# Optimization experiments

Hardware: AMD Instinct MI355X
Metric: run time of the kernel (lower is better)

The kernel has to match this reference:

```python
import jax, jax.numpy as jnp
import numpy as np
import math

SF = 2      # sr_forward
SP = 2      # sr_prior
LAM = 0.05  # lam


def _cubic(x):
    ax = np.abs(x); ax2 = ax * ax; ax3 = ax2 * ax
    return (1.5 * ax3 - 2.5 * ax2 + 1.0) * (ax <= 1) + \
           (-0.5 * ax3 + 2.5 * ax2 - 4.0 * ax + 2.0) * ((ax > 1) & (ax <= 2))


def _weights_indices(in_len, out_len, scale, antialiasing):
    # matlab-style bicubic resample weights (KAIR imresize), computed statically in numpy
    kw = 4.0
    if scale < 1 and antialiasing:
        kw = kw / scale
    x = np.arange(1, out_len + 1, dtype=np.float64)
    u = x / scale + 0.5 * (1.0 - 1.0 / scale)
    left = np.floor(u - kw / 2)
    P = int(math.ceil(kw)) + 2
    ind = left[:, None] + np.arange(P, dtype=np.float64)[None, :]
    dist = u[:, None] - ind
    w = scale * _cubic(dist * scale) if (scale < 1 and antialiasing) else _cubic(dist)
    w = w / w.sum(axis=1, keepdims=True)
    nz = (w == 0).sum(axis=0)
    if nz[0] != 0:
        ind = ind[:, 1:1 + P - 2]; w = w[:, 1:1 + P - 2]
    if nz[-1] != 0:
        ind = ind[:, 0:P - 2]; w = w[:, 0:P - 2]
    sym_s = int(-ind.min() + 1)
    sym_e = int(ind.max() - in_len)
    ind0 = (ind + sym_s - 1).astype(np.int64)  # 0-based into symmetrically padded axis
    return w, ind0, sym_s, sym_e


def imresize(x, scale, antialiasing):
    # x: (C, H, W); faithful matlab bicubic with symmetric boundary padding
    C, H, W = x.shape
    oH, oW = int(math.ceil(H * scale)), int(math.ceil(W * scale))
    wH, iH, sHs, sHe = _weights_indices(H, oH, scale, antialiasing)
    wW, iW, sWs, sWe = _weights_indices(W, oW, scale, antialiasing)
    xp = jnp.pad(x, ((0, 0), (sHs, max(sHe, 0)), (0, 0)), mode='symmetric')
    y = jnp.einsum('chpw,hp->chw', xp[:, iH, :], jnp.asarray(wH, x.dtype))
    yp = jnp.pad(y, ((0, 0), (0, 0), (sWs, max(sWe, 0))), mode='symmetric')
    return jnp.einsum('chwp,wp->chw', yp[:, :, iW], jnp.asarray(wW, x.dtype))


def wrap_conv(x, k):
    # ndimage.convolve(x_HWC, k[...,None], mode='wrap') per channel; k odd-sized (K,K)
    kh, kw = k.shape
    ph, pw = kh // 2, kw // 2
    xp = jnp.pad(x, ((0, 0), (ph, kh - 1 - ph), (pw, kw - 1 - pw)), mode='wrap')
    kf = jnp.flip(k, (0, 1)).astype(x.dtype)[None, None]  # true convolution = corr with flipped kernel
    out = jax.lax.conv_general_dilated(xp[:, None], kf, (1, 1), 'VALID')
    return out[:, 0]


def shift_pixel(x, sf):
    # bilinear (scipy interp2d linear) shift by (sf-1)/2 toward upper-left, clipped at borders
    C, H, W = x.shape
    s = (sf - 1) * 0.5
    yv = np.clip(np.arange(H) + s, 0, H - 1)
    xv = np.clip(np.arange(W) + s, 0, W - 1)
    y0 = np.floor(yv).astype(np.int64); y1 = np.minimum(y0 + 1, H - 1)
    x0 = np.floor(xv).astype(np.int64); x1 = np.minimum(x0 + 1, W - 1)
    wy = jnp.asarray(yv - y0, x.dtype)[None, :, None]
    wx = jnp.asarray(xv - x0, x.dtype)[None, None, :]
    t = x[:, y0, :] * (1 - wy) + x[:, y1, :] * wy
    return t[:, :, x0] * (1 - wx) + t[:, :, x1] * wx


def setup_inputs() -> dict:
    key = jax.random.key(0)
    im = jax.random.normal(key, (1, 3, 2048, 2048), dtype=jnp.float32)
    # 25x25 Gaussian blur kernel (typical SISR forward kernel), normalized to sum 1
    g = np.arange(25) - 12.0
    g = np.exp(-(g ** 2) / (2 * 2.6 ** 2))
    k = np.outer(g, g); k = k / k.sum()
    kernel = jnp.asarray(k, jnp.float32)
    return {"im": im, "kernel": kernel}


def reference(im, kernel):
    x = im[0]                                        # (C, H, W); batch must be 1
    ax = wrap_conv(x, kernel)                        # A: wrap blur
    ax = imresize(ax, 1.0 / SF, False)               # A: downsample (no antialias)
    atax = imresize(ax, float(SF), False)            # A^T: upsample
    atax = wrap_conv(atax, jnp.flip(kernel, (0, 1))) # A^T: conv with flipped kernel
    atax = shift_pixel(atax, SF)                     # A^T: half-pixel alignment shift
    hx = imresize(x, 1.0 / SP, True)                 # H: antialiased downsample
    hthx = imresize(hx, float(SP), True)             # H^T: upsample
    return atax[None] + LAM * hthx[None]             # (1, C, H, W)
```

## Files before the change

kernel.cpp:

```cpp
#include <hip/hip_runtime.h>
#include <math.h>

namespace {

constexpr int W = 2048, H = 2048, NC = 3, HALF = 1024;
constexpr size_t HWSZ = (size_t)W * H;
constexpr size_t MQ = (size_t)HALF * HALF;
constexpr size_t M2 = 2 * MQ;
constexpr float LAM = 0.05f;

__device__ __forceinline__ int refl(int i, int n) {
    return i < 0 ? -1 - i : (i >= n ? 2 * n - 1 - i : i);
}

__global__ void prep(const float* __restrict__ k, float* __restrict__ cf) {
    if (threadIdx.x != 0) return;
    float g[25];
#pragma unroll
    for (int p = 0; p < 25; ++p) { g[p] = sqrtf(k[p * 25 + p]); cf[p] = g[p]; }
    float hw[26];
    hw[0] = 0.5f * g[0];
#pragma unroll
    for (int t = 1; t < 25; ++t) hw[t] = 0.5f * (g[t] + g[t - 1]);
    hw[25] = 0.5f * g[24];
#pragma unroll
    for (int t = 0; t < 26; ++t) cf[32 + t] = hw[t];
#pragma unroll
    for (int d = 0; d < 28; ++d) {
        float s = 0.f;
        if (d < 25) s = fmaf(-0.0625f, g[d], s);
        if (d >= 1 && d <= 25) s = fmaf(0.5625f, g[d - 1], s);
        if (d >= 2 && d <= 26) s = fmaf(0.5625f, g[d - 2], s);
        if (d >= 3) s = fmaf(-0.0625f, g[d - 3], s);
        cf[64 + d] = s;
    }
    const float WE4[4] = {-0.0234375f, 0.2265625f, 0.8671875f, -0.0703125f};
    float C0[17], C1[17];
#pragma unroll
    for (int m = 0; m < 17; ++m) { C0[m] = 0.f; C1[m] = 0.f; }
#pragma unroll
    for (int p = 0; p < 2; ++p) {
#pragma unroll
        for (int t = 0; t < 26; ++t) {
            int r = p - 12 + t;
            int fl = (r + 64) / 2 - 32;
            int e = (r + 64) & 1;
#pragma unroll
            for (int b = 0; b < 4; ++b) {
                int m = fl + e + b - 2 + 8;
                float wub = e ? WE4[3 - b] : WE4[b];
                float add = hw[t] * wub;
                if (p == 0) C0[m] += add;
                else C1[m] += add;
            }
        }
    }
#pragma unroll
    for (int m = 0; m < 17; ++m) { cf[96 + m] = C0[m]; cf[128 + m] = C1[m]; }
}

__global__ __launch_bounds__(256) void front(const float* __restrict__ x,
                                             float* __restrict__ d1,
                                             float* __restrict__ hx,
                                             const float* __restrict__ cf) {
    __shared__ float xs[90][97];
    __shared__ float th[90][33];
    int b = blockIdx.x;
    int tx = b & 31, ty = (b >> 5) & 31, c = b >> 10;
    int tid = threadIdx.x;
    const int r0 = 64 * ty - 13;
    const int c0 = 64 * tx - 16;
    const float* xb = x + (size_t)c * HWSZ;
    {
        int lane8 = tid & 7;
        int rsub = tid >> 3;
#pragma unroll
        for (int rp = 0; rp < 3; ++rp) {
            int r = rp * 32 + rsub;
            if (r < 90) {
                const float* xr = xb + (size_t)((r0 + r) & 2047) * W;
#pragma unroll
                for (int g4 = 0; g4 < 3; ++g4) {
                    int cc = g4 * 8 + lane8;
                    float4 v = *(const float4*)(xr + ((c0 + 4 * cc) & 2047));
                    xs[r][4 * cc + 0] = v.x; xs[r][4 * cc + 1] = v.y;
                    xs[r][4 * cc + 2] = v.z; xs[r][4 * cc + 3] = v.w;
                }
            }
        }
    }
    float g[25], cw[28];
#pragma unroll
    for (int p = 0; p < 25; ++p) g[p] = cf[p];
#pragma unroll
    for (int d = 0; d < 28; ++d) cw[d] = cf[64 + d];
    const bool BROW = (ty == 0 || ty == 31);
    const bool BCOL = (tx == 0 || tx == 31);
    __syncthreads();

    const float WA[8] = {-0.01171875f, -0.03515625f, 0.11328125f, 0.43359375f,
                         0.43359375f,  0.11328125f,  -0.03515625f, -0.01171875f};
    const int ob_r0 = 64 * ty - 3, ob_c0 = 64 * tx - 3;
    for (int idx = tid; idx < 560; idx += 256) {
        int rr = idx >> 3, q = idx & 7;
        int lr = BROW ? (refl(ob_r0 + rr, H) - r0) : (rr + 10);
        const float* xr = &xs[lr][0];
        float a0 = 0.f, a1 = 0.f, a2 = 0.f, a3 = 0.f;
        if (!BCOL) {
            const float* xp = xr + 13 + 8 * q;
#pragma unroll
            for (int u = 0; u < 14; ++u) {
                float v = xp[u];
                if (u < 8) a0 = fmaf(WA[u], v, a0);
                if (u >= 2 && u < 10) a1 = fmaf(WA[u - 2], v, a1);
                if (u >= 4 && u < 12) a2 = fmaf(WA[u - 4], v, a2);
                if (u >= 6) a3 = fmaf(WA[u - 6], v, a3);
            }
        } else {
#pragma unroll
            for (int u = 0; u < 14; ++u) {
                float v = xr[refl(ob_c0 + 8 * q + u, W) - c0];
                if (u < 8) a0 = fmaf(WA[u], v, a0);
                if (u >= 2 && u < 10) a1 = fmaf(WA[u - 2], v, a1);
                if (u >= 4 && u < 12) a2 = fmaf(WA[u - 4], v, a2);
                if (u >= 6) a3 = fmaf(WA[u - 6], v, a3);
            }
        }
        th[rr][4 * q + 0] = a0;
        th[rr][4 * q + 1] = a1;
        th[rr][4 * q + 2] = a2;
        th[rr][4 * q + 3] = a3;
    }
    __syncthreads();
    {
        int oc = tid & 31, og = tid >> 5;
        float a0 = 0.f, a1 = 0.f, a2 = 0.f, a3 = 0.f;
#pragma unroll
        for (int u = 0; u < 14; ++u) {
            float v = th[8 * og + u][oc];
            if (u < 8) a0 = fmaf(WA[u], v, a0);
            if (u >= 2 && u < 10) a1 = fmaf(WA[u - 2], v, a1);
            if (u >= 4 && u < 12) a2 = fmaf(WA[u - 4], v, a2);
            if (u >= 6) a3 = fmaf(WA[u - 6], v, a3);
        }
        float* hp = hx + (size_t)c * MQ + (size_t)(32 * ty + 4 * og) * HALF + 32 * tx + oc;
        hp[0] = a0; hp[HALF] = a1; hp[2 * HALF] = a2; hp[3 * HALF] = a3;
    }
    __syncthreads();

    for (int idx = tid; idx < 720; idx += 256) {
        int r = idx >> 3, q = idx & 7;
        const float* xp = &xs[r][8 * q + 3];
        float a0 = 0.f, a1 = 0.f, a2 = 0.f, a3 = 0.f;
#pragma unroll
        for (int u = 0; u < 34; ++u) {
            float v = xp[u];
            if (u < 28) a0 = fmaf(cw[u], v, a0);
            if (u >= 2 && u < 30) a1 = fmaf(cw[u - 2], v, a1);
            if (u >= 4 && u < 32) a2 = fmaf(cw[u - 4], v, a2);
            if (u >= 6) a3 = fmaf(cw[u - 6], v, a3);
        }
        th[r][4 * q + 0] = a0;
        th[r][4 * q + 1] = a1;
        th[r][4 * q + 2] = a2;
        th[r][4 * q + 3] = a3;
    }
    __syncthreads();
    if (tx == 0) {
        for (int r = tid; r < 90; r += 256) {
            float b0 = 0.f, b1 = 0.f, b2 = 0.f;
#pragma unroll
            for (int p = 0; p < 25; ++p) {
                b0 = fmaf(g[p], xs[r][p + 4], b0);
                b1 = fmaf(g[p], xs[r][p + 5], b1);
                b2 = fmaf(g[p], xs[r][p + 6], b2);
            }
            th[r][0] = 0.5f * b0 + 0.5625f * b1 - 0.0625f * b2;
        }
    }
    if (tx == 31) {
        for (int r = tid; r < 90; r += 256) {
            float b0 = 0.f, b1 = 0.f, b2 = 0.f;
#pragma unroll
            for (int p = 0; p < 25; ++p) {
                b0 = fmaf(g[p], xs[r][p + 65], b0);
                b1 = fmaf(g[p], xs[r][p + 66], b1);
                b2 = fmaf(g[p], xs[r][p + 67], b2);
            }
            th[r][31] = -0.0625f * b0 + 0.5625f * b1 + 0.5f * b2;
        }
    }
    __syncthreads();

    {
        int oc = tid & 31, og = tid >> 5;
        float a0 = 0.f, a1 = 0.f, a2 = 0.f, a3 = 0.f;
#pragma unroll
        for (int u = 0; u < 34; ++u) {
            float v = th[8 * og + u][oc];
            if (u < 28) a0 = fmaf(cw[u], v, a0);
            if (u >= 2 && u < 30) a1 = fmaf(cw[u - 2], v, a1);
            if (u >= 4 && u < 32) a2 = fmaf(cw[u - 4], v, a2);
            if (u >= 6) a3 = fmaf(cw[u - 6], v, a3);
        }
        float av[4] = {a0, a1, a2, a3};
        if (ty == 0 && og == 0) {
            float b0 = 0.f, b1 = 0.f, b2 = 0.f;
#pragma unroll
            for (int p = 0; p < 25; ++p) {
                b0 = fmaf(g[p], th[1 + p][oc], b0);
                b1 = fmaf(g[p], th[2 + p][oc], b1);
                b2 = fmaf(g[p], th[3 + p][oc], b2);
            }
            av[0] = 0.5f * b0 + 0.5625f * b1 - 0.0625f * b2;
        }
        if (ty == 31 && og == 7) {
            float b0 = 0.f, b1 = 0.f, b2 = 0.f;
#pragma unroll
            for (int p = 0; p < 25; ++p) {
                b0 = fmaf(g[p], th[62 + p][oc], b0);
                b1 = fmaf(g[p], th[63 + p][oc], b1);
                b2 = fmaf(g[p], th[64 + p][oc], b2);
            }
            av[3] = -0.0625f * b0 + 0.5625f * b1 + 0.5f * b2;
        }
        float* dp = d1 + (size_t)c * MQ + (size_t)(32 * ty + 4 * og) * HALF + 32 * tx + oc;
#pragma unroll
        for (int k = 0; k < 4; ++k) dp[(size_t)k * HALF] = av[k];
    }
}

__global__ __launch_bounds__(256) void aK(const float* __restrict__ d1,
                                          float* __restrict__ m1,
                                          const float* __restrict__ cf) {
    int b = blockIdx.x;
    int tid = threadIdx.x;
    if (b < 256 * NC) {
        int ib = b & 255, c = b >> 8;
        if (ib < 2 || ib > 253) return;
        float C0[17], C1[17];
#pragma unroll
        for (int m = 0; m < 17; ++m) { C0[m] = cf[96 + m]; C1[m] = cf[128 + m]; }
        int i0 = 8 * ib, q0 = 4 * ib;
        const float* dp = d1 + ((size_t)c * MQ + (size_t)(q0 - 8) * HALF + 4 * tid);
        float4 acc[8];
#pragma unroll
        for (int k = 0; k < 8; ++k) acc[k] = make_float4(0.f, 0.f, 0.f, 0.f);
#pragma unroll
        for (int d = 0; d < 20; ++d) {
            float4 v = *(const float4*)(dp + (size_t)d * HALF);
#pragma unroll
            for (int k = 0; k < 8; ++k) {
                int m = d - (k >> 1);
                if (m >= 0 && m < 17) {
                    float wgt = (k & 1) ? C1[m] : C0[m];
                    acc[k].x = fmaf(wgt, v.x, acc[k].x);
                    acc[k].y = fmaf(wgt, v.y, acc[k].y);
                    acc[k].z = fmaf(wgt, v.z, acc[k].z);
                    acc[k].w = fmaf(wgt, v.w, acc[k].w);
                }
            }
        }
        float* mp = m1 + (size_t)c * M2 + (size_t)i0 * HALF + 4 * tid;
#pragma unroll
        for (int k = 0; k < 8; ++k) *(float4*)(mp + (size_t)k * HALF) = acc[k];
    } else {
        int bid = b - 256 * NC;
        int ri = bid & 31, c = bid >> 5;
        int i = ri < 16 ? ri : 2016 + ri;
        float g[25], hw[26];
#pragma unroll
        for (int p = 0; p < 25; ++p) g[p] = cf[p];
#pragma unroll
        for (int t = 0; t < 26; ++t) hw[t] = cf[32 + t];
        const float WE4[4] = {-0.0234375f, 0.2265625f, 0.8671875f, -0.0703125f};
        bool cl = (i == 2047);
        const float* db = d1 + (size_t)c * MQ + 4 * tid;
        float4 a = make_float4(0.f, 0.f, 0.f, 0.f);
#pragma unroll
        for (int t = 0; t < 26; ++t) {
            float wgt = cl ? (t < 25 ? g[t] : 0.f) : hw[t];
            int ip = (i - 12 + t) & 2047;
            int e = ip & 1, qq = (ip >> 1) + e - 2;
            float4 uv = make_float4(0.f, 0.f, 0.f, 0.f);
#pragma unroll
            for (int bq = 0; bq < 4; ++bq) {
                float wu = e ? WE4[3 - bq] : WE4[bq];
                int rr = refl(qq + bq, HALF);
                float4 v = *(const float4*)(db + (size_t)rr * HALF);
                uv.x = fmaf(wu, v.x, uv.x);
                uv.y = fmaf(wu, v.y, uv.y);
                uv.z = fmaf(wu, v.z, uv.z);
                uv.w = fmaf(wu, v.w, uv.w);
            }
            a.x = fmaf(wgt, uv.x, a.x);
            a.y = fmaf(wgt, uv.y, a.y);
            a.z = fmaf(wgt, uv.z, a.z);
            a.w = fmaf(wgt, uv.w, a.w);
        }
        *(float4*)(m1 + (size_t)c * M2 + (size_t)i * HALF + 4 * tid) = a;
    }
}

__global__ __launch_bounds__(256) void bK(const float* __restrict__ m1,
                                          const float* __restrict__ hx,
                                          float* __restrict__ out,
                                          const float* __restrict__ cf) {
    __shared__ float mr[4][1040];
    __shared__ float hv[4][1040];
    int b = blockIdx.x;
    int tid = threadIdx.x;
    const float WE4[4] = {-0.0234375f, 0.2265625f, 0.8671875f, -0.0703125f};
    if (b < 512 * NC) {
        int rb = b & 511, c = b >> 9;
        float C0[17], C1[17];
#pragma unroll
        for (int m = 0; m < 17; ++m) { C0[m] = cf[96 + m]; C1[m] = cf[128 + m]; }
        int i0 = 4 * rb;
        const float* mb = m1 + (size_t)c * M2 + (size_t)i0 * HALF;
#pragma unroll
        for (int r = 0; r < 4; ++r) {
            float4 v = *(const float4*)(mb + (size_t)r * HALF + 4 * tid);
            *(float4*)&mr[r][8 + 4 * tid] = v;
        }
        const float* hb = hx + (size_t)c * MQ;
        int q2 = 2 * rb;
#pragma unroll
        for (int k = 0; k < 4; ++k) {
            float4 a = make_float4(0.f, 0.f, 0.f, 0.f);
#pragma unroll
            for (int aq = 0; aq < 4; ++aq) {
                float wu = (k & 1) ? WE4[3 - aq] : WE4[aq];
                int row = refl(q2 - 2 + (k >> 1) + (k & 1) + aq, HALF);
                float4 v = *(const float4*)(hb + (size_t)row * HALF + 4 * tid);
                a.x = fmaf(wu, v.x, a.x);
                a.y = fmaf(wu, v.y, a.y);
                a.z = fmaf(wu, v.z, a.z);
                a.w = fmaf(wu, v.w, a.w);
            }
            *(float4*)&hv[k][4 + 4 * tid] = a;
            if (tid == 0) { hv[k][3] = a.x; hv[k][2] = a.y; }
            if (tid == 255) { hv[k][4 + 1024] = a.w; hv[k][4 + 1025] = a.z; }
        }
        __syncthreads();
        bool dostore = (tid >= 2 && tid <= 253);
        float* ob = out + (size_t)c * HWSZ + (size_t)i0 * W + 8 * tid;
#pragma unroll
        for (int r = 0; r < 4; ++r) {
            float w[20];
#pragma unroll
            for (int q5 = 0; q5 < 5; ++q5)
                *(float4*)&w[4 * q5] = *(const float4*)&mr[r][4 * tid + 4 * q5];
            float wv[12];
#pragma unroll
            for (int q3 = 0; q3 < 3; ++q3)
                *(float4*)&wv[4 * q3] = *(const float4*)&hv[r][4 * tid + 4 * q3];
            float res[8];
#pragma unroll
            for (int s = 0; s < 8; ++s) {
                int h = s >> 1;
                float a = 0.f;
#pragma unroll
                for (int m = 0; m < 17; ++m)
                    a = fmaf((s & 1) ? C1[m] : C0[m], w[h + m], a);
                float uh = 0.f;
#pragma unroll
                for (int bq = 0; bq < 4; ++bq)
                    uh = fmaf((s & 1) ? WE4[3 - bq] : WE4[bq], wv[h + (s & 1) + 2 + bq], uh);
                res[s] = fmaf(LAM, uh, a);
            }
            if (dostore) {
                *(float4*)(ob + (size_t)r * W) = make_float4(res[0], res[1], res[2], res[3]);
                *(float4*)(ob + (size_t)r * W + 4) = make_float4(res[4], res[5], res[6], res[7]);
            }
        }
    } else {
        int bid = b - 512 * NC;
        int rg = bid & 255, c = bid >> 8;
        int i = 8 * rg + (tid >> 5);
        int cc = tid & 31;
        int j = cc < 16 ? cc : 2016 + cc;
        float g[25], hw[26];
#pragma unroll
        for (int p = 0; p < 25; ++p) g[p] = cf[p];
#pragma unroll
        for (int t = 0; t < 26; ++t) hw[t] = cf[32 + t];
        const float* mrow = m1 + (size_t)c * M2 + (size_t)i * HALF;
        bool cl = (j == 2047);
        float val = 0.f;
#pragma unroll
        for (int t = 0; t < 26; ++t) {
            float wgt = cl ? (t < 25 ? g[t] : 0.f) : hw[t];
            int jp = (j - 12 + t) & 2047;
            int e = jp & 1;
            int qq = (jp >> 1) + e - 2;
            float uh = 0.f;
#pragma unroll
            for (int bq = 0; bq < 4; ++bq)
                uh = fmaf(e ? WE4[3 - bq] : WE4[bq], mrow[refl(qq + bq, HALF)], uh);
            val = fmaf(wgt, uh, val);
        }
        const float* hb = hx + (size_t)c * MQ;
        int qi = (i >> 1) + (i & 1) - 2;
        int qj = (j >> 1) + (j & 1) - 2;
        float hval = 0.f;
#pragma unroll
        for (int aq = 0; aq < 4; ++aq) {
            const float* hr = hb + (size_t)refl(qi + aq, HALF) * HALF;
            float rowa = (i & 1) ? WE4[3 - aq] : WE4[aq];
            float s = 0.f;
#pragma unroll
            for (int bq = 0; bq < 4; ++bq)
                s = fmaf((j & 1) ? WE4[3 - bq] : WE4[bq], hr[refl(qj + bq, HALF)], s);
            hval = fmaf(rowa, s, hval);
        }
        out[(size_t)c * HWSZ + (size_t)i * W + j] = fmaf(LAM, hval, val);
    }
}

}

extern "C" void kernel_launch(void* const* d_in, const int* in_sizes, int n_in,
                              void* d_out, int out_size, void* d_ws, size_t ws_size,
                              hipStream_t stream) {
    (void)in_sizes; (void)n_in; (void)out_size; (void)ws_size;
    const float* x = (const float*)d_in[0];
    const float* k = (const float*)d_in[1];
    float* ws = (float*)d_ws;
    float* out = (float*)d_out;

    float* hxp = ws;
    float* d1 = hxp + 3 * MQ;
    float* m1 = d1 + 3 * MQ;
    float* cf = m1 + 3 * M2;

    hipLaunchKernelGGL(prep, dim3(1), dim3(32), 0, stream, k, cf);
    hipLaunchKernelGGL(front, dim3(32 * 32 * NC), dim3(256), 0, stream, x, d1, hxp, cf);
    hipLaunchKernelGGL(aK, dim3(256 * NC + 32 * NC), dim3(256), 0, stream, d1, m1, cf);
    hipLaunchKernelGGL(bK, dim3(512 * NC + 256 * NC), dim3(256), 0, stream, m1, hxp, out, cf);
}
```

Before: 162.8 us.

## Fuse interior vertical pass into output kernel and vectorize front LDS reads

The interior vertical 17-tap pass that aK wrote to m1 now runs inside bK2 on shared-memory tiles loaded from d1, so the m1 round trip for interior rows goes away. aK2 now computes only the border columns, and the row-boundary quads fall back to the old row-quad path. The front kernel's horizontal convolutions read shared memory as float4 vectors into registers, with xs padded to 100 columns for alignment. The cost is heavier shared-memory use per block, redundant halo loads, and more complex boundary logic.

```diff
diff --git a/kernel.cpp b/kernel.cpp
--- a/kernel.cpp
+++ b/kernel.cpp
@@ -11,6 +11,9 @@
 
 __device__ __forceinline__ int refl(int i, int n) {
     return i < 0 ? -1 - i : (i >= n ? 2 * n - 1 - i : i);
+}
+__device__ __forceinline__ int iclamp(int v, int lo, int hi) {
+    return v < lo ? lo : (v > hi ? hi : v);
 }
 
 __global__ void prep(const float* __restrict__ k, float* __restrict__ cf) {
@@ -63,7 +66,7 @@
                                              float* __restrict__ d1,
                                              float* __restrict__ hx,
                                              const float* __restrict__ cf) {
-    __shared__ float xs[90][97];
+    __shared__ float xs[90][100];
     __shared__ float th[90][33];
     int b = blockIdx.x;
     int tx = b & 31, ty = (b >> 5) & 31, c = b >> 10;
@@ -83,8 +86,7 @@
                 for (int g4 = 0; g4 < 3; ++g4) {
                     int cc = g4 * 8 + lane8;
                     float4 v = *(const float4*)(xr + ((c0 + 4 * cc) & 2047));
-                    xs[r][4 * cc + 0] = v.x; xs[r][4 * cc + 1] = v.y;
-                    xs[r][4 * cc + 2] = v.z; xs[r][4 * cc + 3] = v.w;
+                    *(float4*)&xs[r][4 * cc] = v;
                 }
             }
         }
@@ -107,14 +109,16 @@
         const float* xr = &xs[lr][0];
         float a0 = 0.f, a1 = 0.f, a2 = 0.f, a3 = 0.f;
         if (!BCOL) {
-            const float* xp = xr + 13 + 8 * q;
-#pragma unroll
-            for (int u = 0; u < 14; ++u) {
-                float v = xp[u];
-                if (u < 8) a0 = fmaf(WA[u], v, a0);
-                if (u >= 2 && u < 10) a1 = fmaf(WA[u - 2], v, a1);
-                if (u >= 4 && u < 12) a2 = fmaf(WA[u - 4], v, a2);
-                if (u >= 6) a3 = fmaf(WA[u - 6], v, a3);
+            float xw[16];
+#pragma unroll
+            for (int v4 = 0; v4 < 4; ++v4)
+                *(float4*)&xw[4 * v4] = *(const float4*)(xr + 8 * q + 12 + 4 * v4);
+#pragma unroll
+            for (int u = 0; u < 8; ++u) {
+                a0 = fmaf(WA[u], xw[u + 1], a0);
+                a1 = fmaf(WA[u], xw[u + 3], a1);
+                a2 = fmaf(WA[u], xw[u + 5], a2);
+                a3 = fmaf(WA[u], xw[u + 7], a3);
             }
         } else {
 #pragma unroll
@@ -150,15 +154,18 @@
 
     for (int idx = tid; idx < 720; idx += 256) {
         int r = idx >> 3, q = idx & 7;
-        const float* xp = &xs[r][8 * q + 3];
+        float xw[40];
+#pragma unroll
+        for (int v4 = 0; v4 < 10; ++v4)
+            *(float4*)&xw[4 * v4] = *(const float4*)(&xs[r][8 * q] + 4 * v4);
         float a0 = 0.f, a1 = 0.f, a2 = 0.f, a3 = 0.f;
 #pragma unroll
-        for (int u = 0; u < 34; ++u) {
-            float v = xp[u];
-            if (u < 28) a0 = fmaf(cw[u], v, a0);
-            if (u >= 2 && u < 30) a1 = fmaf(cw[u - 2], v, a1);
-            if (u >= 4 && u < 32) a2 = fmaf(cw[u - 4], v, a2);
-            if (u >= 6) a3 = fmaf(cw[u - 6], v, a3);
+        for (int u = 0; u < 28; ++u) {
+            float w = cw[u];
+            a0 = fmaf(w, xw[u + 3], a0);
+            a1 = fmaf(w, xw[u + 5], a1);
+            a2 = fmaf(w, xw[u + 7], a2);
+            a3 = fmaf(w, xw[u + 9], a3);
         }
         th[r][4 * q + 0] = a0;
         th[r][4 * q + 1] = a1;
@@ -230,42 +237,40 @@
     }
 }
 
-__global__ __launch_bounds__(256) void aK(const float* __restrict__ d1,
-                                          float* __restrict__ m1,
-                                          const float* __restrict__ cf) {
+__global__ __launch_bounds__(256) void aK2(const float* __restrict__ d1,
+                                           float* __restrict__ m1,
+                                           const float* __restrict__ cf) {
+    __shared__ float ds2[24][68];
     int b = blockIdx.x;
     int tid = threadIdx.x;
-    if (b < 256 * NC) {
-        int ib = b & 255, c = b >> 8;
-        if (ib < 2 || ib > 253) return;
+    if (b < 126 * NC) {
+        int c = b / 126, ib = b - 126 * c;
+        int i0 = 16 + 16 * ib;
+        int q0m = (i0 >> 1) - 8;
+        int cc = tid & 63;
+        int qcol = cc < 32 ? cc : 960 + cc;
+        const float* d1c = d1 + (size_t)c * MQ;
+        for (int r = tid >> 6; r < 24; r += 4)
+            ds2[r][cc] = d1c[(size_t)(q0m + r) * HALF + qcol];
+        __syncthreads();
         float C0[17], C1[17];
 #pragma unroll
         for (int m = 0; m < 17; ++m) { C0[m] = cf[96 + m]; C1[m] = cf[128 + m]; }
-        int i0 = 8 * ib, q0 = 4 * ib;
-        const float* dp = d1 + ((size_t)c * MQ + (size_t)(q0 - 8) * HALF + 4 * tid);
-        float4 acc[8];
-#pragma unroll
-        for (int k = 0; k < 8; ++k) acc[k] = make_float4(0.f, 0.f, 0.f, 0.f);
-#pragma unroll
-        for (int d = 0; d < 20; ++d) {
-            float4 v = *(const float4*)(dp + (size_t)d * HALF);
-#pragma unroll
-            for (int k = 0; k < 8; ++k) {
-                int m = d - (k >> 1);
-                if (m >= 0 && m < 17) {
-                    float wgt = (k & 1) ? C1[m] : C0[m];
-                    acc[k].x = fmaf(wgt, v.x, acc[k].x);
-                    acc[k].y = fmaf(wgt, v.y, acc[k].y);
-                    acc[k].z = fmaf(wgt, v.z, acc[k].z);
-                    acc[k].w = fmaf(wgt, v.w, acc[k].w);
-                }
-            }
-        }
-        float* mp = m1 + (size_t)c * M2 + (size_t)i0 * HALF + 4 * tid;
-#pragma unroll
-        for (int k = 0; k < 8; ++k) *(float4*)(mp + (size_t)k * HALF) = acc[k];
+        float* mc = m1 + (size_t)c * M2;
+        int rbase = (tid >> 6) * 4;
+#pragma unroll
+        for (int k = 0; k < 4; ++k) {
+            int rr = rbase + k;
+            float a = 0.f;
+#pragma unroll
+            for (int m = 0; m < 17; ++m) {
+                float wgt = (rr & 1) ? C1[m] : C0[m];
+                a = fmaf(wgt, ds2[(rr >> 1) + m][cc], a);
+            }
+            mc[(size_t)(i0 + rr) * HALF + qcol] = a;
+        }
     } else {
-        int bid = b - 256 * NC;
+        int bid = b - 126 * NC;
         int ri = bid & 31, c = bid >> 5;
         int i = ri < 16 ? ri : 2016 + ri;
         float g[25], hw[26];
@@ -302,80 +307,181 @@
     }
 }
 
-__global__ __launch_bounds__(256) void bK(const float* __restrict__ m1,
-                                          const float* __restrict__ hx,
-                                          float* __restrict__ out,
-                                          const float* __restrict__ cf) {
-    __shared__ float mr[4][1040];
-    __shared__ float hv[4][1040];
+__device__ __forceinline__ void bk_rowquad(int i0, int c,
+                                           const float* __restrict__ m1,
+                                           const float* __restrict__ hx,
+                                           float* __restrict__ out,
+                                           const float* __restrict__ cf,
+                                           float* smem, int tid) {
+    float (*mr)[1040] = (float (*)[1040])smem;
+    float (*hv)[1040] = (float (*)[1040])(smem + 4160);
+    const float WE4[4] = {-0.0234375f, 0.2265625f, 0.8671875f, -0.0703125f};
+    float C0[17], C1[17];
+#pragma unroll
+    for (int m = 0; m < 17; ++m) { C0[m] = cf[96 + m]; C1[m] = cf[128 + m]; }
+    const float* mb = m1 + (size_t)c * M2 + (size_t)i0 * HALF;
+#pragma unroll
+    for (int r = 0; r < 4; ++r) {
+        float4 v = *(const float4*)(mb + (size_t)r * HALF + 4 * tid);
+        *(float4*)&mr[r][8 + 4 * tid] = v;
+    }
+    const float* hb = hx + (size_t)c * MQ;
+    int q2 = i0 >> 1;
+#pragma unroll
+    for (int k = 0; k < 4; ++k) {
+        float4 a = make_float4(0.f, 0.f, 0.f, 0.f);
+#pragma unroll
+        for (int aq = 0; aq < 4; ++aq) {
+            float wu = (k & 1) ? WE4[3 - aq] : WE4[aq];
+            int row = refl(q2 - 2 + (k >> 1) + (k & 1) + aq, HALF);
+            float4 v = *(const float4*)(hb + (size_t)row * HALF + 4 * tid);
+            a.x = fmaf(wu, v.x, a.x);
+            a.y = fmaf(wu, v.y, a.y);
+            a.z = fmaf(wu, v.z, a.z);
+            a.w = fmaf(wu, v.w, a.w);
+        }
+        *(float4*)&hv[k][4 + 4 * tid] = a;
+        if (tid == 0) { hv[k][3] = a.x; hv[k][2] = a.y; }
+        if (tid == 255) { hv[k][4 + 1024] = a.w; hv[k][4 + 1025] = a.z; }
+    }
+    __syncthreads();
+    bool dostore = (tid >= 2 && tid <= 253);
+    float* ob = out + (size_t)c * HWSZ + (size_t)i0 * W + 8 * tid;
+#pragma unroll
+    for (int r = 0; r < 4; ++r) {
+        float w[20];
+#pragma unroll
+        for (int q5 = 0; q5 < 5; ++q5)
+            *(float4*)&w[4 * q5] = *(const float4*)&mr[r][4 * tid + 4 * q5];
+        float wv[12];
+#pragma unroll
+        for (int q3 = 0; q3 < 3; ++q3)
+            *(float4*)&wv[4 * q3] = *(const float4*)&hv[r][4 * tid + 4 * q3];
+        float res[8];
+#pragma unroll
+        for (int s = 0; s < 8; ++s) {
+            int h = s >> 1;
+            float a = 0.f;
+#pragma unroll
+            for (int m = 0; m < 17; ++m)
+                a = fmaf((s & 1) ? C1[m] : C0[m], w[h + m], a);
+            float uh = 0.f;
+#pragma unroll
+            for (int bq = 0; bq < 4; ++bq)
+                uh = fmaf((s & 1) ? WE4[3 - bq] : WE4[bq], wv[h + (s & 1) + 2 + bq], uh);
+            res[s] = fmaf(LAM, uh, a);
+        }
+        if (dostore) {
+            *(float4*)(ob + (size_t)r * W) = make_float4(res[0], res[1], res[2], res[3]);
+            *(float4*)(ob + (size_t)r * W + 4) = make_float4(res[4], res[5], res[6], res[7]);
+        }
+    }
+}
+
+__global__ __launch_bounds__(256) void bK2(const float* __restrict__ d1,
+                                           const float* __restrict__ m1,
+                                           const float* __restrict__ hx,
+                                           float* __restrict__ out,
+                                           const float* __restrict__ cf) {
+    __shared__ float smem[12192];
     int b = blockIdx.x;
     int tid = threadIdx.x;
     const float WE4[4] = {-0.0234375f, 0.2265625f, 0.8671875f, -0.0703125f};
     if (b < 512 * NC) {
-        int rb = b & 511, c = b >> 9;
+        int c = b >> 9;
+        int r2 = b & 511;
+        int cb = r2 >> 6, rb = r2 & 63;
+        int i0 = 32 * rb, j0 = 256 * cb;
+        int q0 = 16 * rb, h0 = 128 * cb;
+        float* dsp = smem;
+        float* msp = smem + 4736;
+        float* hsp = smem + 9472;
+        float* hvp = smem;
+        const float* d1c = d1 + (size_t)c * MQ;
+        const float* hxc = hx + (size_t)c * MQ;
+        for (int idx = tid; idx < 1152; idx += 256) {
+            int r = idx / 36, s = idx - 36 * r;
+            int grow = iclamp(q0 - 8 + r, 0, 1023);
+            int gcol = iclamp(h0 - 8 + 4 * s, 0, 1020);
+            *(float4*)(dsp + r * 148 + 4 * s) = *(const float4*)(d1c + (size_t)grow * HALF + gcol);
+        }
+        for (int idx = tid; idx < 2640; idx += 256) {
+            int r = idx / 132, cc = idx - 132 * r;
+            int grow = iclamp(q0 - 2 + r, 0, 1023);
+            int gcol = iclamp(h0 - 2 + cc, 0, 1023);
+            hsp[r * 136 + cc] = hxc[(size_t)grow * HALF + gcol];
+        }
         float C0[17], C1[17];
 #pragma unroll
         for (int m = 0; m < 17; ++m) { C0[m] = cf[96 + m]; C1[m] = cf[128 + m]; }
-        int i0 = 4 * rb;
-        const float* mb = m1 + (size_t)c * M2 + (size_t)i0 * HALF;
-#pragma unroll
-        for (int r = 0; r < 4; ++r) {
-            float4 v = *(const float4*)(mb + (size_t)r * HALF + 4 * tid);
-            *(float4*)&mr[r][8 + 4 * tid] = v;
-        }
-        const float* hb = hx + (size_t)c * MQ;
-        int q2 = 2 * rb;
+        __syncthreads();
+        for (int idx = tid; idx < 4608; idx += 256) {
+            int r = idx / 144, cc = idx - 144 * r;
+            const float* base = dsp + (r >> 1) * 148 + cc;
+            float a = 0.f;
+#pragma unroll
+            for (int m = 0; m < 17; ++m) {
+                float wgt = (r & 1) ? C1[m] : C0[m];
+                a = fmaf(wgt, base[m * 148], a);
+            }
+            msp[r * 148 + cc] = a;
+        }
+        __syncthreads();
+        for (int idx = tid; idx < 4224; idx += 256) {
+            int r = idx / 132, cc = idx - 132 * r;
+            const float* hb2 = hsp + ((r >> 1) + (r & 1)) * 136 + cc;
+            float a = 0.f;
+#pragma unroll
+            for (int aq = 0; aq < 4; ++aq) {
+                float wgt = (r & 1) ? WE4[3 - aq] : WE4[aq];
+                a = fmaf(wgt, hb2[aq * 136], a);
+            }
+            hvp[r * 136 + cc] = a;
+        }
+        __syncthreads();
+        int jg = tid & 31, rg = tid >> 5;
+        int j = j0 + 8 * jg;
+        bool pcol = (j >= 16) && (j <= 2024);
+        float* outc = out + (size_t)c * HWSZ;
 #pragma unroll
         for (int k = 0; k < 4; ++k) {
-            float4 a = make_float4(0.f, 0.f, 0.f, 0.f);
-#pragma unroll
-            for (int aq = 0; aq < 4; ++aq) {
-                float wu = (k & 1) ? WE4[3 - aq] : WE4[aq];
-                int row = refl(q2 - 2 + (k >> 1) + (k & 1) + aq, HALF);
-                float4 v = *(const float4*)(hb + (size_t)row * HALF + 4 * tid);
-                a.x = fmaf(wu, v.x, a.x);
-                a.y = fmaf(wu, v.y, a.y);
-                a.z = fmaf(wu, v.z, a.z);
-                a.w = fmaf(wu, v.w, a.w);
-            }
-            *(float4*)&hv[k][4 + 4 * tid] = a;
-            if (tid == 0) { hv[k][3] = a.x; hv[k][2] = a.y; }
-            if (tid == 255) { hv[k][4 + 1024] = a.w; hv[k][4 + 1025] = a.z; }
-        }
-        __syncthreads();
-        bool dostore = (tid >= 2 && tid <= 253);
-        float* ob = out + (size_t)c * HWSZ + (size_t)i0 * W + 8 * tid;
-#pragma unroll
-        for (int r = 0; r < 4; ++r) {
-            float w[20];
+            int r = rg + 8 * k;
+            int i = i0 + r;
+            float w20[20];
 #pragma unroll
             for (int q5 = 0; q5 < 5; ++q5)
-                *(float4*)&w[4 * q5] = *(const float4*)&mr[r][4 * tid + 4 * q5];
-            float wv[12];
-#pragma unroll
-            for (int q3 = 0; q3 < 3; ++q3)
-                *(float4*)&wv[4 * q3] = *(const float4*)&hv[r][4 * tid + 4 * q3];
+                *(float4*)&w20[4 * q5] = *(const float4*)(msp + r * 148 + 4 * jg + 4 * q5);
+            float wv8[8];
+#pragma unroll
+            for (int q2v = 0; q2v < 2; ++q2v)
+                *(float4*)&wv8[4 * q2v] = *(const float4*)(hvp + r * 136 + 4 * jg + 4 * q2v);
             float res[8];
 #pragma unroll
             for (int s = 0; s < 8; ++s) {
-                int h = s >> 1;
+                int hh = s >> 1;
                 float a = 0.f;
 #pragma unroll
                 for (int m = 0; m < 17; ++m)
-                    a = fmaf((s & 1) ? C1[m] : C0[m], w[h + m], a);
+                    a = fmaf((s & 1) ? C1[m] : C0[m], w20[hh + m], a);
                 float uh = 0.f;
 #pragma unroll
                 for (int bq = 0; bq < 4; ++bq)
-                    uh = fmaf((s & 1) ? WE4[3 - bq] : WE4[bq], wv[h + (s & 1) + 2 + bq], uh);
+                    uh = fmaf((s & 1) ? WE4[3 - bq] : WE4[bq], wv8[hh + (s & 1) + bq], uh);
                 res[s] = fmaf(LAM, uh, a);
             }
-            if (dostore) {
-                *(float4*)(ob + (size_t)r * W) = make_float4(res[0], res[1], res[2], res[3]);
-                *(float4*)(ob + (size_t)r * W + 4) = make_float4(res[4], res[5], res[6], res[7]);
-            }
-        }
+            if (pcol && i >= 16 && i < 2032) {
+                float* ob = outc + (size_t)i * W + j;
+                *(float4*)ob = make_float4(res[0], res[1], res[2], res[3]);
+                *(float4*)(ob + 4) = make_float4(res[4], res[5], res[6], res[7]);
+            }
+        }
+    } else if (b < 512 * NC + 8 * NC) {
+        int t = b - 512 * NC;
+        int c = t >> 3, k = t & 7;
+        int i0 = (k < 4) ? 4 * k : 2016 + 4 * k;
+        bk_rowquad(i0, c, m1, hx, out, cf, smem, tid);
     } else {
-        int bid = b - 512 * NC;
+        int bid = b - (512 * NC + 8 * NC);
         int rg = bid & 255, c = bid >> 8;
         int i = 8 * rg + (tid >> 5);
         int cc = tid & 31;
@@ -384,14 +490,14 @@
 #pragma unroll
         for (int p = 0; p < 25; ++p) g[p] = cf[p];
 #pragma unroll
-        for (int t = 0; t < 26; ++t) hw[t] = cf[32 + t];
+        for (int t2 = 0; t2 < 26; ++t2) hw[t2] = cf[32 + t2];
         const float* mrow = m1 + (size_t)c * M2 + (size_t)i * HALF;
         bool cl = (j == 2047);
         float val = 0.f;
 #pragma unroll
-        for (int t = 0; t < 26; ++t) {
-            float wgt = cl ? (t < 25 ? g[t] : 0.f) : hw[t];
-            int jp = (j - 12 + t) & 2047;
+        for (int t2 = 0; t2 < 26; ++t2) {
+            float wgt = cl ? (t2 < 25 ? g[t2] : 0.f) : hw[t2];
+            int jp = (j - 12 + t2) & 2047;
             int e = jp & 1;
             int qq = (jp >> 1) + e - 2;
             float uh = 0.f;
@@ -436,6 +542,7 @@
 
     hipLaunchKernelGGL(prep, dim3(1), dim3(32), 0, stream, k, cf);
     hipLaunchKernelGGL(front, dim3(32 * 32 * NC), dim3(256), 0, stream, x, d1, hxp, cf);
-    hipLaunchKernelGGL(aK, dim3(256 * NC + 32 * NC), dim3(256), 0, stream, d1, m1, cf);
-    hipLaunchKernelGGL(bK, dim3(512 * NC + 256 * NC), dim3(256), 0, stream, m1, hxp, out, cf);
-}
+    hipLaunchKernelGGL(aK2, dim3(126 * NC + 32 * NC), dim3(256), 0, stream, d1, m1, cf);
+    hipLaunchKernelGGL(bK2, dim3(512 * NC + 8 * NC + 256 * NC), dim3(256), 0, stream,
+                       d1, m1, hxp, out, cf);
+}
```

Result: slower. 170.7 us (+4.9%).
